# Performance work log

Hardware: AMD Instinct MI355X
Metric: run time of the kernel (lower is better)

The kernel has to match this reference:

```python
import jax, jax.numpy as jnp
import numpy as np

N_NODES = 50000

def gcn_conv(x, edge_index, W, b):
    # PyG GCNConv default: add self-loops, symmetric norm D^-1/2 (A+I) D^-1/2, then XW + b
    n = x.shape[0]
    loop = jnp.arange(n, dtype=edge_index.dtype)
    src = jnp.concatenate([edge_index[0], loop])
    dst = jnp.concatenate([edge_index[1], loop])
    deg = jax.ops.segment_sum(jnp.ones_like(src, dtype=x.dtype), dst, num_segments=n)
    dinv = jnp.where(deg > 0, jax.lax.rsqrt(jnp.maximum(deg, 1e-12)), 0.0)
    norm = dinv[src] * dinv[dst]                      # [E+N]
    h = x @ W                                          # [N, d_out]
    msg = h[src] * norm[:, None]                       # gather + scale
    out = jax.ops.segment_sum(msg, dst, num_segments=n)  # scatter-add
    return out + b

def leaky(x):
    return jnp.where(x >= 0, x, 0.01 * x)

def setup_inputs() -> dict:
    key = jax.random.key(0)
    ks = jax.random.split(key, 10)
    x = jax.random.normal(ks[0], (N_NODES, 128), dtype=jnp.float32)
    edge_index = jax.random.randint(ks[1], (2, 800000), 0, N_NODES, dtype=jnp.int64)
    W1 = jax.random.normal(ks[2], (128, 512), dtype=jnp.float32) / np.sqrt(128)
    b1 = jnp.zeros((512,), dtype=jnp.float32)
    W3 = jax.random.normal(ks[3], (512, 128), dtype=jnp.float32) / np.sqrt(512)
    b3 = jnp.zeros((128,), dtype=jnp.float32)
    fc1_w = jax.random.normal(ks[4], (256, 128), dtype=jnp.float32) * np.sqrt(2.0 / 256)
    fc1_b = jnp.zeros((256,), dtype=jnp.float32)
    fc2_w = jax.random.normal(ks[5], (1, 256), dtype=jnp.float32) * np.sqrt(2.0 / 1)
    fc2_b = jnp.zeros((1,), dtype=jnp.float32)
    return {"x": x, "edge_index": edge_index, "W1": W1, "b1": b1, "W3": W3, "b3": b3,
            "fc1_w": fc1_w, "fc1_b": fc1_b, "fc2_w": fc2_w, "fc2_b": fc2_b}

def reference(x, edge_index, W1, b1, W3, b3, fc1_w, fc1_b, fc2_w, fc2_b):
    h = leaky(gcn_conv(x, edge_index, W1, b1))
    h = leaky(gcn_conv(h, edge_index, W3, b3))
    h = leaky(h @ fc1_w.T + fc1_b)
    h = h @ fc2_w.T + fc2_b
    return h.squeeze(-1)  # [N]
```

## Files before the change

### kernel.cpp

```cpp
#include <hip/hip_runtime.h>
#include <hip/hip_fp16.h>

typedef _Float16 f16x8 __attribute__((ext_vector_type(8)));
typedef __attribute__((ext_vector_type(4))) float f32x4;

static __device__ __forceinline__ float leaky(float v) { return v >= 0.f ? v : 0.01f * v; }

__global__ __launch_bounds__(256) void k_prep_all(
    const float* __restrict__ x, const float* __restrict__ W1, const float* __restrict__ W3,
    const float* __restrict__ fc1w, const float* __restrict__ fc2b,
    const int* __restrict__ dst, int* __restrict__ bucket_cnt,
    float* __restrict__ out, __half* __restrict__ x16,
    _Float16* __restrict__ W1f, _Float16* __restrict__ W3f, _Float16* __restrict__ F1f,
    int N, int E)
{
    __shared__ int bcnt[256];
    bcnt[threadIdx.x] = 0;
    __syncthreads();
    const int gsz = gridDim.x * 256;
    const int gtid = blockIdx.x * 256 + threadIdx.x;
    float ob = fc2b[0];
    for (int i = gtid; i < N; i += gsz) out[i] = ob;
    for (int i = gtid; i < 32 * 4 * 64 * 8; i += gsz) {
        int j = i & 7, l = (i >> 3) & 63, ks = (i >> 9) & 3, cb = i >> 11;
        int k = ks * 32 + (l >> 4) * 8 + j, n = cb * 16 + (l & 15);
        W1f[i] = (_Float16)W1[k * 512 + n];
    }
    for (int i = gtid; i < 8 * 16 * 64 * 8; i += gsz) {
        int j = i & 7, l = (i >> 3) & 63, ks = (i >> 9) & 15, cb = i >> 13;
        int k = ks * 32 + (l >> 4) * 8 + j, n = cb * 16 + (l & 15);
        W3f[i] = (_Float16)W3[k * 128 + n];
    }
    for (int i = gtid; i < 16 * 4 * 64 * 8; i += gsz) {
        int j = i & 7, l = (i >> 3) & 63, ks = (i >> 9) & 3, cb = i >> 11;
        int k = ks * 32 + (l >> 4) * 8 + j, n = cb * 16 + (l & 15);
        F1f[i] = (_Float16)fc1w[n * 128 + k];
    }
    for (int i = gtid; i < N * 64; i += gsz) {
        float2 f = ((const float2*)x)[i];
        ((__half2*)x16)[i] = __floats2half2_rn(f.x, f.y);
    }
    for (int e = gtid; e < E; e += gsz) atomicAdd(&bcnt[dst[e] >> 8], 1);
    __syncthreads();
    int c = bcnt[threadIdx.x];
    if (c > 0) atomicAdd(&bucket_cnt[threadIdx.x], c);
}

__global__ __launch_bounds__(256) void k_bscan(const int* __restrict__ bucket_cnt,
                                               int* __restrict__ bucket_base,
                                               int* __restrict__ bucket_cursor,
                                               int* __restrict__ rowptr, int N, int E) {
    __shared__ int s[256];
    int tx = threadIdx.x;
    int v = bucket_cnt[tx];
    s[tx] = v; __syncthreads();
    for (int off = 1; off < 256; off <<= 1) {
        int t = (tx >= off) ? s[tx - off] : 0;
        __syncthreads();
        s[tx] += t;
        __syncthreads();
    }
    int excl = s[tx] - v;
    bucket_base[tx] = excl;
    bucket_cursor[tx] = excl;
    if (tx == 0) { bucket_base[256] = E; rowptr[N] = E; }
}

__global__ __launch_bounds__(256) void k_bfill(const int* __restrict__ src, const int* __restrict__ dst,
                                               int* __restrict__ bucket_cursor,
                                               unsigned int* __restrict__ pairs, int E) {
    __shared__ int cnt[256];
    __shared__ int base[256];
    const int CH = 4096;
    int c0 = blockIdx.x * CH;
    int cend = c0 + CH < E ? c0 + CH : E;
    int tx = threadIdx.x;
    cnt[tx] = 0;
    __syncthreads();
    for (int i = c0 + tx; i < cend; i += 256) atomicAdd(&cnt[dst[i] >> 8], 1);
    __syncthreads();
    int myc = cnt[tx];
    int mybase = 0;
    if (myc > 0) mybase = atomicAdd(&bucket_cursor[tx], myc);
    __syncthreads();
    cnt[tx] = 0;
    base[tx] = mybase;
    __syncthreads();
    for (int i = c0 + tx; i < cend; i += 256) {
        int d = dst[i];
        int b = d >> 8;
        int pos = base[b] + atomicAdd(&cnt[b], 1);
        pairs[pos] = ((unsigned)(d & 255) << 24) | (unsigned)src[i];
    }
}

__global__ __launch_bounds__(256) void k_bsort(const unsigned int* __restrict__ pairs,
                                               const int* __restrict__ bucket_base,
                                               int* __restrict__ rowptr, float* __restrict__ dinv,
                                               int* __restrict__ csr, __half* __restrict__ x16,
                                               int N) {
    __shared__ int cnt[256], pre[256], cur[64];
    __shared__ float sdinv[256];
    __shared__ int stage[3072];
    const int B = blockIdx.x >> 2, q = blockIdx.x & 3;
    const int tx = threadIdx.x;
    const int pbase = bucket_base[B], pcnt = bucket_base[B + 1] - pbase;
    cnt[tx] = 0;
    __syncthreads();
    for (int i = tx; i < pcnt; i += 256) atomicAdd(&cnt[pairs[pbase + i] >> 24], 1);
    __syncthreads();
    int v = cnt[tx];
    pre[tx] = v; __syncthreads();
    for (int off = 1; off < 256; off <<= 1) {
        int t = (tx >= off) ? pre[tx - off] : 0;
        __syncthreads();
        pre[tx] += t;
        __syncthreads();
    }
    float dv = rsqrtf((float)v + 1.0f);
    sdinv[tx] = dv;
    int node = B * 256 + tx;
    if (node < N) {
        rowptr[node] = pbase + (pre[tx] - v);
        dinv[node] = dv;
    }
    const int d0 = q * 64;
    const int qstart = pre[d0] - cnt[d0];
    const int qcnt = pre[d0 + 63] - qstart;
    if (tx < 64) cur[tx] = (pre[d0 + tx] - cnt[d0 + tx]) - qstart;
    __syncthreads();
    if (qcnt > 0) {
        if (qcnt <= 3072) {
            for (int i = tx; i < pcnt; i += 256) {
                unsigned p = pairs[pbase + i];
                int dl = (int)(p >> 24) - d0;
                if ((unsigned)dl < 64u) {
                    int pos = atomicAdd(&cur[dl], 1);
                    stage[pos] = (int)(p & 0xFFFFFFu);
                }
            }
            __syncthreads();
            for (int i = tx; i < qcnt; i += 256) csr[pbase + qstart + i] = stage[i];
        } else {
            for (int i = tx; i < pcnt; i += 256) {
                unsigned p = pairs[pbase + i];
                int dl = (int)(p >> 24) - d0;
                if ((unsigned)dl < 64u) {
                    int pos = atomicAdd(&cur[dl], 1);
                    csr[pbase + qstart + pos] = (int)(p & 0xFFFFFFu);
                }
            }
        }
    }
    for (int i = tx; i < 64 * 64; i += 256) {
        int r = i >> 6, c = i & 63;
        int nd = B * 256 + q * 64 + r;
        if (nd < N) {
            float s = sdinv[q * 64 + r];
            float2 f = __half22float2(((__half2*)x16)[nd * 64 + c]);
            ((__half2*)x16)[nd * 64 + c] = __floats2half2_rn(f.x * s, f.y * s);
        }
    }
}

template <bool BIASACT>
__global__ __launch_bounds__(256) void k_gather(const __half* __restrict__ X,
                                                const int* __restrict__ rowptr,
                                                const int* __restrict__ csr,
                                                const float* __restrict__ dinv,
                                                const float* __restrict__ bias,
                                                __half* __restrict__ outp, int N) {
    int wid = __builtin_amdgcn_readfirstlane((int)((blockIdx.x * 256 + threadIdx.x) >> 6));
    if (wid >= N) return;
    int lane = threadIdx.x & 63, c = lane * 2;
    float di = dinv[wid];
    float2 self = __half22float2(*(const __half2*)(X + (size_t)wid * 128 + c));
    float accx = self.x, accy = self.y;
    int k = rowptr[wid], end = rowptr[wid + 1];
    for (; k < end; k += 8) {
        int ss[8];
        #pragma unroll
        for (int i = 0; i < 8; ++i) {
            int idx = k + i;
            ss[i] = (idx < end) ? csr[idx] : -1;
        }
        #pragma unroll
        for (int i = 0; i < 8; ++i) {
            if (ss[i] >= 0) {
                float2 f = __half22float2(*(const __half2*)(X + (size_t)ss[i] * 128 + c));
                accx += f.x;
                accy += f.y;
            }
        }
    }
    accx *= di;
    accy *= di;
    if (BIASACT) {
        accx = leaky(accx + bias[c]);
        accy = leaky(accy + bias[c + 1]);
    }
    *(__half2*)(outp + (size_t)wid * 128 + c) = __floats2half2_rn(accx, accy);
}

__global__ __launch_bounds__(256, 2) void k_fused12(
    const __half* __restrict__ A1h, const _Float16* __restrict__ W1f,
    const _Float16* __restrict__ W3f, const float* __restrict__ b1,
    const float* __restrict__ dinv, __half* __restrict__ t2, int M)
{
    __shared__ __align__(16) _Float16 As[128 * 136];
    __shared__ __align__(16) _Float16 Hs[128 * 136];
    const int tid = threadIdx.x, lane = tid & 63, wid = tid >> 6;
    const int wr = wid >> 1, wc = wid & 1;
    const int m0 = blockIdx.x * 128;
    {
        const int r = tid >> 1, hf = tid & 1;
        int gr = m0 + r; if (gr >= M) gr = M - 1;
        const __half* Ar = A1h + (size_t)gr * 128;
        #pragma unroll
        for (int c = 0; c < 8; ++c) {
            int ch = hf * 8 + c;
            *(uint4*)(As + r * 136 + ch * 8) = *(const uint4*)(Ar + ch * 8);
        }
    }
    float bq[4][4];
    #pragma unroll
    for (int q = 0; q < 4; ++q)
        #pragma unroll
        for (int n = 0; n < 4; ++n)
            bq[q][n] = b1[q * 128 + wc * 64 + n * 16 + (lane & 15)];
    __syncthreads();

    const int arow = lane & 15, kch = (lane >> 4) * 8;
    f32x4 acc2[4][4] = {};
    #pragma unroll
    for (int q = 0; q < 4; ++q) {
        f32x4 acc1[4][4] = {};
        #pragma unroll
        for (int ks = 0; ks < 4; ++ks) {
            f16x8 af[4], bf[4];
            #pragma unroll
            for (int i = 0; i < 4; ++i)
                af[i] = *(const f16x8*)(As + (wr * 64 + i * 16 + arow) * 136 + ks * 32 + kch);
            #pragma unroll
            for (int n = 0; n < 4; ++n) {
                int cb = q * 8 + wc * 4 + n;
                bf[n] = *(const f16x8*)(W1f + ((size_t)(cb * 4 + ks) * 64 + lane) * 8);
            }
            #pragma unroll
            for (int i = 0; i < 4; ++i)
                #pragma unroll
                for (int n = 0; n < 4; ++n)
                    acc1[i][n] = __builtin_amdgcn_mfma_f32_16x16x32_f16(af[i], bf[n], acc1[i][n], 0, 0, 0);
        }
        __syncthreads();
        #pragma unroll
        for (int i = 0; i < 4; ++i)
            #pragma unroll
            for (int n = 0; n < 4; ++n)
                #pragma unroll
                for (int j = 0; j < 4; ++j) {
                    int row = wr * 64 + i * 16 + (lane >> 4) * 4 + j;
                    int col = wc * 64 + n * 16 + (lane & 15);
                    Hs[row * 136 + col] = (_Float16)leaky(acc1[i][n][j] + bq[q][n]);
                }
        __syncthreads();
        #pragma unroll
        for (int ks = 0; ks < 4; ++ks) {
            f16x8 af[4], bf[4];
            #pragma unroll
            for (int i = 0; i < 4; ++i)
                af[i] = *(const f16x8*)(Hs + (wr * 64 + i * 16 + arow) * 136 + ks * 32 + kch);
            #pragma unroll
            for (int n = 0; n < 4; ++n) {
                int cb = wc * 4 + n, ksg = q * 4 + ks;
                bf[n] = *(const f16x8*)(W3f + ((size_t)(cb * 16 + ksg) * 64 + lane) * 8);
            }
            #pragma unroll
            for (int i = 0; i < 4; ++i)
                #pragma unroll
                for (int n = 0; n < 4; ++n)
                    acc2[i][n] = __builtin_amdgcn_mfma_f32_16x16x32_f16(af[i], bf[n], acc2[i][n], 0, 0, 0);
        }
    }
    __syncthreads();
    #pragma unroll
    for (int i = 0; i < 4; ++i)
        #pragma unroll
        for (int j = 0; j < 4; ++j) {
            int row = wr * 64 + i * 16 + (lane >> 4) * 4 + j;
            int gr = m0 + row;
            float dv = dinv[gr < M ? gr : M - 1];
            #pragma unroll
            for (int n = 0; n < 4; ++n) {
                int col = wc * 64 + n * 16 + (lane & 15);
                Hs[row * 136 + col] = (_Float16)(acc2[i][n][j] * dv);
            }
        }
    __syncthreads();
    {
        const int r = tid >> 1, hf = tid & 1;
        int gr = m0 + r;
        if (gr < M) {
            #pragma unroll
            for (int c = 0; c < 8; ++c) {
                int ch = hf * 8 + c;
                *(uint4*)(t2 + (size_t)gr * 128 + ch * 8) = *(const uint4*)(Hs + r * 136 + ch * 8);
            }
        }
    }
}

__global__ __launch_bounds__(256, 2) void k_fgemm3(
    const __half* __restrict__ A3h, const _Float16* __restrict__ F1f,
    const float* __restrict__ fc1b, const float* __restrict__ fc2w,
    float* __restrict__ out, int M)
{
    __shared__ __align__(16) _Float16 As[128 * 136];
    const int tid = threadIdx.x, lane = tid & 63, wid = tid >> 6;
    const int wr = wid >> 1, wc = wid & 1;
    const int bx = blockIdx.x & 1, m0 = (blockIdx.x >> 1) * 128;
    const int nbase = bx * 128;
    {
        const int r = tid >> 1, hf = tid & 1;
        int gr = m0 + r; if (gr >= M) gr = M - 1;
        const __half* Ar = A3h + (size_t)gr * 128;
        #pragma unroll
        for (int c = 0; c < 8; ++c) {
            int ch = hf * 8 + c;
            *(uint4*)(As + r * 136 + ch * 8) = *(const uint4*)(Ar + ch * 8);
        }
    }
    __syncthreads();
    const int arow = lane & 15, kch = (lane >> 4) * 8;
    f32x4 acc[4][4] = {};
    #pragma unroll
    for (int ks = 0; ks < 4; ++ks) {
        f16x8 af[4], bf[4];
        #pragma unroll
        for (int i = 0; i < 4; ++i)
            af[i] = *(const f16x8*)(As + (wr * 64 + i * 16 + arow) * 136 + ks * 32 + kch);
        #pragma unroll
        for (int n = 0; n < 4; ++n) {
            int cb = bx * 8 + wc * 4 + n;
            bf[n] = *(const f16x8*)(F1f + ((size_t)(cb * 4 + ks) * 64 + lane) * 8);
        }
        #pragma unroll
        for (int i = 0; i < 4; ++i)
            #pragma unroll
            for (int n = 0; n < 4; ++n)
                acc[i][n] = __builtin_amdgcn_mfma_f32_16x16x32_f16(af[i], bf[n], acc[i][n], 0, 0, 0);
    }
    #pragma unroll
    for (int i = 0; i < 4; ++i)
        #pragma unroll
        for (int j = 0; j < 4; ++j) {
            int row = m0 + wr * 64 + i * 16 + (lane >> 4) * 4 + j;
            float s = 0.f;
            #pragma unroll
            for (int n = 0; n < 4; ++n) {
                int col = nbase + wc * 64 + n * 16 + (lane & 15);
                float v = leaky(acc[i][n][j] + fc1b[col]);
                s += v * fc2w[col];
            }
            s += __shfl_xor(s, 8);
            s += __shfl_xor(s, 4);
            s += __shfl_xor(s, 2);
            s += __shfl_xor(s, 1);
            if ((lane & 15) == 0 && row < M) atomicAdd(&out[row], s);
        }
}

extern "C" void kernel_launch(void* const* d_in, const int* in_sizes, int n_in,
                              void* d_out, int out_size, void* d_ws, size_t ws_size,
                              hipStream_t stream) {
    const float* x    = (const float*)d_in[0];
    const int*   ei   = (const int*)d_in[1];
    const float* W1   = (const float*)d_in[2];
    const float* b1   = (const float*)d_in[3];
    const float* W3   = (const float*)d_in[4];
    const float* b3   = (const float*)d_in[5];
    const float* fc1w = (const float*)d_in[6];
    const float* fc1b = (const float*)d_in[7];
    const float* fc2w = (const float*)d_in[8];
    const float* fc2b = (const float*)d_in[9];
    float* out = (float*)d_out;

    int N = in_sizes[0] / 128;
    int E = in_sizes[1] / 2;
    const int* src = ei;
    const int* dst = ei + E;

    char* ws = (char*)d_ws;
    size_t off = 0;
    auto alloc = [&](size_t bytes) { void* p = ws + off; off += (bytes + 255) & ~255ull; return p; };
    int*   bucket_cnt    = (int*)alloc(257 * 4);
    int*   bucket_base   = (int*)alloc(257 * 4);
    int*   bucket_cursor = (int*)alloc(257 * 4);
    int*   rowptr = (int*)alloc((size_t)(N + 1) * 4);
    unsigned int* pairs = (unsigned int*)alloc((size_t)E * 4);
    int*   csr    = (int*)alloc((size_t)E * 4);
    float* dinv   = (float*)alloc((size_t)N * 4);
    __half* x16   = (__half*)alloc((size_t)N * 128 * 2);
    __half* A1h   = (__half*)alloc((size_t)N * 128 * 2);
    __half* t2    = (__half*)alloc((size_t)N * 128 * 2);
    __half* A3h   = (__half*)alloc((size_t)N * 128 * 2);
    _Float16* W1f = (_Float16*)alloc((size_t)32 * 4 * 64 * 8 * 2);
    _Float16* W3f = (_Float16*)alloc((size_t)8 * 16 * 64 * 8 * 2);
    _Float16* F1f = (_Float16*)alloc((size_t)16 * 4 * 64 * 8 * 2);
    (void)ws_size; (void)n_in; (void)out_size;

    const int MB128 = (N + 127) / 128;
    const int NB = (N + 255) >> 8;
    dim3 blk(256);

    hipMemsetAsync(bucket_cnt, 0, 257 * 4, stream);

    k_prep_all<<<1024, blk, 0, stream>>>(x, W1, W3, fc1w, fc2b, dst, bucket_cnt,
                                         out, x16, W1f, W3f, F1f, N, E);
    k_bscan<<<1, blk, 0, stream>>>(bucket_cnt, bucket_base, bucket_cursor, rowptr, N, E);
    k_bfill<<<(E + 4095) / 4096, blk, 0, stream>>>(src, dst, bucket_cursor, pairs, E);
    k_bsort<<<NB * 4, blk, 0, stream>>>(pairs, bucket_base, rowptr, dinv, csr, x16, N);
    k_gather<false><<<(N * 64 + 255) / 256, blk, 0, stream>>>(x16, rowptr, csr, dinv, nullptr, A1h, N);
    k_fused12<<<MB128, blk, 0, stream>>>(A1h, W1f, W3f, b1, dinv, t2, N);
    k_gather<true><<<(N * 64 + 255) / 256, blk, 0, stream>>>(t2, rowptr, csr, dinv, b3, A3h, N);
    k_fgemm3<<<MB128 * 2, blk, 0, stream>>>(A3h, F1f, fc1b, fc2w, out, N);
}
```

Before: 298.5 us.

## Pad CSR rows to multiples of eight with self-loop and zero-row sentinels

Each CSR row now holds the self-loop entry and is padded up to a multiple of eight with a sentinel index N that points at an extra all-zero row appended to x16 and t2. Per-node info (row start, iteration count, dinv) is packed into one uint4 descriptor, replacing the rowptr and dinv loads. The gather loop drops its bounds checks and predicated loads and runs a fixed count of unconditional 8-wide iterations. In exchange it does extra padded loads (on average about 3.5 per row), uses more CSR memory, and the sort kernel gets a larger shared staging buffer.

```diff
diff --git a/kernel.cpp b/kernel.cpp
--- a/kernel.cpp
+++ b/kernel.cpp
@@ -10,7 +10,7 @@
     const float* __restrict__ x, const float* __restrict__ W1, const float* __restrict__ W3,
     const float* __restrict__ fc1w, const float* __restrict__ fc2b,
     const int* __restrict__ dst, int* __restrict__ bucket_cnt,
-    float* __restrict__ out, __half* __restrict__ x16,
+    float* __restrict__ out, __half* __restrict__ x16, __half* __restrict__ t2,
     _Float16* __restrict__ W1f, _Float16* __restrict__ W3f, _Float16* __restrict__ F1f,
     int N, int E)
 {
@@ -21,6 +21,10 @@
     const int gtid = blockIdx.x * 256 + threadIdx.x;
     float ob = fc2b[0];
     for (int i = gtid; i < N; i += gsz) out[i] = ob;
+    for (int i = gtid; i < 64; i += gsz) {
+        ((__half2*)x16)[(size_t)N * 64 + i] = __floats2half2_rn(0.f, 0.f);
+        ((__half2*)t2)[(size_t)N * 64 + i] = __floats2half2_rn(0.f, 0.f);
+    }
     for (int i = gtid; i < 32 * 4 * 64 * 8; i += gsz) {
         int j = i & 7, l = (i >> 3) & 63, ks = (i >> 9) & 3, cb = i >> 11;
         int k = ks * 32 + (l >> 4) * 8 + j, n = cb * 16 + (l & 15);
@@ -48,8 +52,7 @@
 
 __global__ __launch_bounds__(256) void k_bscan(const int* __restrict__ bucket_cnt,
                                                int* __restrict__ bucket_base,
-                                               int* __restrict__ bucket_cursor,
-                                               int* __restrict__ rowptr, int N, int E) {
+                                               int* __restrict__ bucket_cursor, int E) {
     __shared__ int s[256];
     int tx = threadIdx.x;
     int v = bucket_cnt[tx];
@@ -63,7 +66,7 @@
     int excl = s[tx] - v;
     bucket_base[tx] = excl;
     bucket_cursor[tx] = excl;
-    if (tx == 0) { bucket_base[256] = E; rowptr[N] = E; }
+    if (tx == 0) bucket_base[256] = E;
 }
 
 __global__ __launch_bounds__(256) void k_bfill(const int* __restrict__ src, const int* __restrict__ dst,
@@ -96,59 +99,73 @@
 
 __global__ __launch_bounds__(256) void k_bsort(const unsigned int* __restrict__ pairs,
                                                const int* __restrict__ bucket_base,
-                                               int* __restrict__ rowptr, float* __restrict__ dinv,
+                                               uint4* __restrict__ desc, float* __restrict__ dinv,
                                                int* __restrict__ csr, __half* __restrict__ x16,
                                                int N) {
     __shared__ int cnt[256], pre[256], cur[64];
     __shared__ float sdinv[256];
-    __shared__ int stage[3072];
+    __shared__ int stage[3584];
     const int B = blockIdx.x >> 2, q = blockIdx.x & 3;
     const int tx = threadIdx.x;
     const int pbase = bucket_base[B], pcnt = bucket_base[B + 1] - pbase;
+    const int PB = pbase + B * 2048;
     cnt[tx] = 0;
     __syncthreads();
     for (int i = tx; i < pcnt; i += 256) atomicAdd(&cnt[pairs[pbase + i] >> 24], 1);
     __syncthreads();
-    int v = cnt[tx];
-    pre[tx] = v; __syncthreads();
+    int deg = cnt[tx];
+    int cnt8 = (deg + 8) & ~7;
+    float dv = rsqrtf((float)deg + 1.0f);
+    __syncthreads();
+    cnt[tx] = cnt8;
+    sdinv[tx] = dv;
+    pre[tx] = cnt8;
+    __syncthreads();
     for (int off = 1; off < 256; off <<= 1) {
         int t = (tx >= off) ? pre[tx - off] : 0;
         __syncthreads();
         pre[tx] += t;
         __syncthreads();
     }
-    float dv = rsqrtf((float)v + 1.0f);
-    sdinv[tx] = dv;
+    int excl = pre[tx] - cnt8;
     int node = B * 256 + tx;
     if (node < N) {
-        rowptr[node] = pbase + (pre[tx] - v);
+        desc[node] = make_uint4((unsigned)(PB + excl), (unsigned)(cnt8 >> 3),
+                                __float_as_uint(dv), 0u);
         dinv[node] = dv;
     }
+    __syncthreads();
+    pre[tx] = excl;
+    __syncthreads();
     const int d0 = q * 64;
-    const int qstart = pre[d0] - cnt[d0];
-    const int qcnt = pre[d0 + 63] - qstart;
-    if (tx < 64) cur[tx] = (pre[d0 + tx] - cnt[d0 + tx]) - qstart;
-    __syncthreads();
-    if (qcnt > 0) {
-        if (qcnt <= 3072) {
-            for (int i = tx; i < pcnt; i += 256) {
-                unsigned p = pairs[pbase + i];
-                int dl = (int)(p >> 24) - d0;
-                if ((unsigned)dl < 64u) {
-                    int pos = atomicAdd(&cur[dl], 1);
-                    stage[pos] = (int)(p & 0xFFFFFFu);
-                }
-            }
-            __syncthreads();
-            for (int i = tx; i < qcnt; i += 256) csr[pbase + qstart + i] = stage[i];
-        } else {
-            for (int i = tx; i < pcnt; i += 256) {
-                unsigned p = pairs[pbase + i];
-                int dl = (int)(p >> 24) - d0;
-                if ((unsigned)dl < 64u) {
-                    int pos = atomicAdd(&cur[dl], 1);
-                    csr[pbase + qstart + pos] = (int)(p & 0xFFFFFFu);
-                }
+    const int qstart8 = pre[d0];
+    const int qcnt8 = pre[d0 + 63] + cnt[d0 + 63] - qstart8;
+    if (tx < 64) cur[tx] = pre[d0 + tx] - qstart8 + 1;
+    __syncthreads();
+    if (qcnt8 <= 3584) {
+        for (int i = tx; i < qcnt8; i += 256) stage[i] = N;
+        __syncthreads();
+        if (tx < 64) stage[pre[d0 + tx] - qstart8] = B * 256 + d0 + tx;
+        for (int i = tx; i < pcnt; i += 256) {
+            unsigned p = pairs[pbase + i];
+            int dl = (int)(p >> 24) - d0;
+            if ((unsigned)dl < 64u) {
+                int pos = atomicAdd(&cur[dl], 1);
+                stage[pos] = (int)(p & 0xFFFFFFu);
+            }
+        }
+        __syncthreads();
+        for (int i = tx; i < qcnt8; i += 256) csr[PB + qstart8 + i] = stage[i];
+    } else {
+        for (int i = tx; i < qcnt8; i += 256) csr[PB + qstart8 + i] = N;
+        __syncthreads();
+        if (tx < 64) csr[PB + pre[d0 + tx]] = B * 256 + d0 + tx;
+        for (int i = tx; i < pcnt; i += 256) {
+            unsigned p = pairs[pbase + i];
+            int dl = (int)(p >> 24) - d0;
+            if ((unsigned)dl < 64u) {
+                int pos = atomicAdd(&cur[dl], 1);
+                csr[PB + qstart8 + pos] = (int)(p & 0xFFFFFFu);
             }
         }
     }
@@ -157,40 +174,36 @@
         int nd = B * 256 + q * 64 + r;
         if (nd < N) {
             float s = sdinv[q * 64 + r];
-            float2 f = __half22float2(((__half2*)x16)[nd * 64 + c]);
-            ((__half2*)x16)[nd * 64 + c] = __floats2half2_rn(f.x * s, f.y * s);
+            float2 f = __half22float2(((__half2*)x16)[(size_t)nd * 64 + c]);
+            ((__half2*)x16)[(size_t)nd * 64 + c] = __floats2half2_rn(f.x * s, f.y * s);
         }
     }
 }
 
 template <bool BIASACT>
 __global__ __launch_bounds__(256) void k_gather(const __half* __restrict__ X,
-                                                const int* __restrict__ rowptr,
+                                                const uint4* __restrict__ desc,
                                                 const int* __restrict__ csr,
-                                                const float* __restrict__ dinv,
                                                 const float* __restrict__ bias,
                                                 __half* __restrict__ outp, int N) {
     int wid = __builtin_amdgcn_readfirstlane((int)((blockIdx.x * 256 + threadIdx.x) >> 6));
     if (wid >= N) return;
     int lane = threadIdx.x & 63, c = lane * 2;
-    float di = dinv[wid];
-    float2 self = __half22float2(*(const __half2*)(X + (size_t)wid * 128 + c));
-    float accx = self.x, accy = self.y;
-    int k = rowptr[wid], end = rowptr[wid + 1];
-    for (; k < end; k += 8) {
+    uint4 d = desc[wid];
+    int k0 = __builtin_amdgcn_readfirstlane((int)d.x);
+    int nit = __builtin_amdgcn_readfirstlane((int)d.y);
+    float di = __uint_as_float(d.z);
+    float accx = 0.f, accy = 0.f;
+    for (int it = 0; it < nit; ++it) {
+        int kk = k0 + it * 8;
         int ss[8];
         #pragma unroll
+        for (int i = 0; i < 8; ++i) ss[i] = csr[kk + i];
+        #pragma unroll
         for (int i = 0; i < 8; ++i) {
-            int idx = k + i;
-            ss[i] = (idx < end) ? csr[idx] : -1;
-        }
-        #pragma unroll
-        for (int i = 0; i < 8; ++i) {
-            if (ss[i] >= 0) {
-                float2 f = __half22float2(*(const __half2*)(X + (size_t)ss[i] * 128 + c));
-                accx += f.x;
-                accy += f.y;
-            }
+            float2 f = __half22float2(*(const __half2*)(X + (size_t)ss[i] * 128 + c));
+            accx += f.x;
+            accy += f.y;
         }
     }
     accx *= di;
@@ -390,19 +403,20 @@
     const int* src = ei;
     const int* dst = ei + E;
 
+    const int NB = (N + 255) >> 8;
     char* ws = (char*)d_ws;
     size_t off = 0;
     auto alloc = [&](size_t bytes) { void* p = ws + off; off += (bytes + 255) & ~255ull; return p; };
     int*   bucket_cnt    = (int*)alloc(257 * 4);
     int*   bucket_base   = (int*)alloc(257 * 4);
     int*   bucket_cursor = (int*)alloc(257 * 4);
-    int*   rowptr = (int*)alloc((size_t)(N + 1) * 4);
+    uint4* desc   = (uint4*)alloc((size_t)N * 16);
     unsigned int* pairs = (unsigned int*)alloc((size_t)E * 4);
-    int*   csr    = (int*)alloc((size_t)E * 4);
+    int*   csr    = (int*)alloc(((size_t)E + (size_t)NB * 2048) * 4);
     float* dinv   = (float*)alloc((size_t)N * 4);
-    __half* x16   = (__half*)alloc((size_t)N * 128 * 2);
+    __half* x16   = (__half*)alloc((size_t)(N + 1) * 128 * 2);
     __half* A1h   = (__half*)alloc((size_t)N * 128 * 2);
-    __half* t2    = (__half*)alloc((size_t)N * 128 * 2);
+    __half* t2    = (__half*)alloc((size_t)(N + 1) * 128 * 2);
     __half* A3h   = (__half*)alloc((size_t)N * 128 * 2);
     _Float16* W1f = (_Float16*)alloc((size_t)32 * 4 * 64 * 8 * 2);
     _Float16* W3f = (_Float16*)alloc((size_t)8 * 16 * 64 * 8 * 2);
@@ -410,18 +424,17 @@
     (void)ws_size; (void)n_in; (void)out_size;
 
     const int MB128 = (N + 127) / 128;
-    const int NB = (N + 255) >> 8;
     dim3 blk(256);
 
     hipMemsetAsync(bucket_cnt, 0, 257 * 4, stream);
 
     k_prep_all<<<1024, blk, 0, stream>>>(x, W1, W3, fc1w, fc2b, dst, bucket_cnt,
-                                         out, x16, W1f, W3f, F1f, N, E);
-    k_bscan<<<1, blk, 0, stream>>>(bucket_cnt, bucket_base, bucket_cursor, rowptr, N, E);
+                                         out, x16, t2, W1f, W3f, F1f, N, E);
+    k_bscan<<<1, blk, 0, stream>>>(bucket_cnt, bucket_base, bucket_cursor, E);
     k_bfill<<<(E + 4095) / 4096, blk, 0, stream>>>(src, dst, bucket_cursor, pairs, E);
-    k_bsort<<<NB * 4, blk, 0, stream>>>(pairs, bucket_base, rowptr, dinv, csr, x16, N);
-    k_gather<false><<<(N * 64 + 255) / 256, blk, 0, stream>>>(x16, rowptr, csr, dinv, nullptr, A1h, N);
+    k_bsort<<<NB * 4, blk, 0, stream>>>(pairs, bucket_base, desc, dinv, csr, x16, N);
+    k_gather<false><<<(N * 64 + 255) / 256, blk, 0, stream>>>(x16, desc, csr, nullptr, A1h, N);
     k_fused12<<<MB128, blk, 0, stream>>>(A1h, W1f, W3f, b1, dinv, t2, N);
-    k_gather<true><<<(N * 64 + 255) / 256, blk, 0, stream>>>(t2, rowptr, csr, dinv, b3, A3h, N);
+    k_gather<true><<<(N * 64 + 255) / 256, blk, 0, stream>>>(t2, desc, csr, b3, A3h, N);
     k_fgemm3<<<MB128 * 2, blk, 0, stream>>>(A3h, F1f, fc1b, fc2w, out, N);
 }
```

Measured after the change: 246.8 us. -17.3%, faster.
